# Kernel tuning notes

Measured on AMD Instinct MI355X. Metric: run time of the kernel, lower is better.

Reference implementation:

```python
import jax, jax.numpy as jnp
import numpy as np

N = 50000   # nodes per modality sub-graph
M = 20000   # hyperedges per modality
E = 200000  # incidences per modality
D = 128     # kg_emb_dim
H = 8       # mha_n_heads
C = 64      # context entities
NE = 200000 # n_entity


def hyper_conv(x, theta, bias, node_idx, edge_idx, num_edges):
    """PyG HypergraphConv (no attention): out = D^-1 H B^-1 H^T (X Theta) + b."""
    xt = x @ theta                                   # [N, D]
    n = x.shape[0]
    ones = jnp.ones(node_idx.shape, dtype=xt.dtype)
    B = jax.ops.segment_sum(ones, edge_idx, num_segments=num_edges)   # edge degree [M]
    Dn = jax.ops.segment_sum(ones, node_idx, num_segments=n)          # node degree [N]
    Binv = jnp.where(B > 0, 1.0 / B, 0.0)
    Dinv = jnp.where(Dn > 0, 1.0 / Dn, 0.0)
    e = jax.ops.segment_sum(xt[node_idx], edge_idx, num_segments=num_edges) * Binv[:, None]
    out = jax.ops.segment_sum(e[edge_idx], node_idx, num_segments=n) * Dinv[:, None]
    return out + bias


def mha(q_in, kv, wq, bq, wk, bk, wv, bv, wo, bo, n_heads):
    """torch.nn.MultiheadAttention(batch_first) with batch=1: query=[C,D], kv=[R,D]."""
    c, d = q_in.shape
    r = kv.shape[0]
    hd = d // n_heads
    q = (q_in @ wq + bq).reshape(c, n_heads, hd).transpose(1, 0, 2)   # [H,C,hd]
    k = (kv @ wk + bk).reshape(r, n_heads, hd).transpose(1, 0, 2)     # [H,R,hd]
    v = (kv @ wv + bv).reshape(r, n_heads, hd).transpose(1, 0, 2)     # [H,R,hd]
    scores = jnp.einsum('hcd,hrd->hcr', q, k) / jnp.sqrt(jnp.asarray(hd, q.dtype))
    attn = jax.nn.softmax(scores, axis=-1)
    o = jnp.einsum('hcr,hrd->hcd', attn, v)                           # [H,C,hd]
    o = o.transpose(1, 0, 2).reshape(c, d)
    return o @ wo + bo


def setup_inputs() -> dict:
    key = jax.random.key(0)
    ks = jax.random.split(key, 24)
    s = D ** -0.5
    inp = {
        'x_item': jax.random.normal(ks[0], (N, D), jnp.float32) * s,
        'theta_item': jax.random.normal(ks[1], (D, D), jnp.float32) * s,
        'bias_item': jnp.zeros((D,), jnp.float32),
        'x_ent': jax.random.normal(ks[2], (N, D), jnp.float32) * s,
        'theta_ent': jax.random.normal(ks[3], (D, D), jnp.float32) * s,
        'bias_ent': jnp.zeros((D,), jnp.float32),
        'x_word': jax.random.normal(ks[4], (N, D), jnp.float32) * s,
        'theta_word': jax.random.normal(ks[5], (D, D), jnp.float32) * s,
        'bias_word': jnp.zeros((D,), jnp.float32),
        'context': jax.random.normal(ks[6], (C, D), jnp.float32),
        'wq': jax.random.normal(ks[7], (D, D), jnp.float32) * s,
        'bq': jnp.zeros((D,), jnp.float32),
        'wk': jax.random.normal(ks[8], (D, D), jnp.float32) * s,
        'bk': jnp.zeros((D,), jnp.float32),
        'wv': jax.random.normal(ks[9], (D, D), jnp.float32) * s,
        'bv': jnp.zeros((D,), jnp.float32),
        'wo': jax.random.normal(ks[10], (D, D), jnp.float32) * s,
        'bo': jnp.zeros((D,), jnp.float32),
        'w_rec': jax.random.normal(ks[11], (D, NE), jnp.float32) * s,
        'b_rec': jnp.zeros((NE,), jnp.float32),
        'node_item': jax.random.randint(ks[12], (E,), 0, N, jnp.int32),
        'edge_item': jax.random.randint(ks[13], (E,), 0, M, jnp.int32),
        'node_ent': jax.random.randint(ks[14], (E,), 0, N, jnp.int32),
        'edge_ent': jax.random.randint(ks[15], (E,), 0, M, jnp.int32),
        'node_word': jax.random.randint(ks[16], (E,), 0, N, jnp.int32),
        'edge_word': jax.random.randint(ks[17], (E,), 0, M, jnp.int32),
        'num_edges': M,
    }
    return inp


def reference(x_item, theta_item, bias_item, x_ent, theta_ent, bias_ent,
              x_word, theta_word, bias_word, context,
              wq, bq, wk, bk, wv, bv, wo, bo, w_rec, b_rec,
              node_item, edge_item, node_ent, edge_ent, node_word, edge_word,
              num_edges):
    # Hypergraph conv per modality (item / entity / word sub-graphs)
    item_emb = hyper_conv(x_item, theta_item, bias_item, node_item, edge_item, num_edges)
    ent_emb = hyper_conv(x_ent, theta_ent, bias_ent, node_ent, edge_ent, num_edges)
    word_emb = hyper_conv(x_word, theta_word, bias_word, node_word, edge_word, num_edges)
    # related = cat(session_embedding, knowledge_embedding) across modalities
    related = jnp.concatenate([item_emb, ent_emb, word_emb], axis=0)   # [3N, D]
    # MHItemAttention: MHA(context, related, related)
    attentive = mha(context, related, wq, bq, wk, bk, wv, bv, wo, bo, H)  # [C, D]
    # Mean pooling path of _attention_and_gating
    user_repr = jnp.mean(attentive, axis=0)                            # [D]
    user_repr = jnp.mean(jnp.concatenate([context, user_repr[None]], axis=0), axis=0)
    # rec_bias: Linear(kg_emb_dim, n_entity)
    scores = user_repr @ w_rec + b_rec                                 # [n_entity]
    return scores
```

## Files before the change

### kernel.cpp

```cpp
#include <hip/hip_runtime.h>
#include <hip/hip_bf16.h>

constexpr int N_NODES = 50000;
constexpr int M_EDGES = 20000;
constexpr int E_INC   = 200000;
constexpr int H_HEADS = 8;
constexpr int C_CTX   = 64;
constexpr int NE_OUT  = 200000;
constexpr int R_REL   = 3 * N_NODES;

constexpr int STRIPS  = 128;
constexpr int SROWS   = 1172;

constexpr int CAP_E = 40;
constexpr int CAP_N = 24;

typedef short bf8v __attribute__((ext_vector_type(8)));
typedef float f4v  __attribute__((ext_vector_type(4)));
#define MFMA16(a, b, c) __builtin_amdgcn_mfma_f32_16x16x32_bf16(a, b, c, 0, 0, 0)

__device__ __forceinline__ unsigned short bfs(float f) {
    union { __hip_bfloat16 b; unsigned short s; } u;
    u.b = __float2bfloat16(f);
    return u.s;
}
__device__ __forceinline__ unsigned bfp(float lo, float hi) {
    union { __hip_bfloat162 b; unsigned u; } v;
    v.b = __float22bfloat162_rn(make_float2(lo, hi));
    return v.u;
}

__device__ __forceinline__ void gload16(const void* g, const void* l) {
    __builtin_amdgcn_global_load_lds(
        (const __attribute__((address_space(1))) void*)(unsigned long long)(size_t)g,
        (__attribute__((address_space(3))) void*)(unsigned)(size_t)l,
        16, 0, 0);
}

__global__ __launch_bounds__(256) void zero_kernel(float4* p, int n4) {
    int i = blockIdx.x * 256 + threadIdx.x;
    if (i < n4) p[i] = make_float4(0.f, 0.f, 0.f, 0.f);
}

__global__ __launch_bounds__(256) void wconv_kernel(
    const float* __restrict__ t0, const float* __restrict__ t1,
    const float* __restrict__ t2, unsigned short* __restrict__ out)
{
    int idx = blockIdx.x * 256 + threadIdx.x;
    int m = idx >> 14, p = idx & 16383;
    int n = p >> 7, k = p & 127;
    const float* src = (m == 0) ? t0 : (m == 1) ? t1 : t2;
    out[idx] = bfs(src[k * 128 + n]);
}

__global__ __launch_bounds__(256) void qkf_kernel(
    const float* __restrict__ ctx, const float* __restrict__ wq,
    const float* __restrict__ bq, const float* __restrict__ wk,
    const float* __restrict__ bk, unsigned short* __restrict__ qkb,
    float* __restrict__ cb)
{
    __shared__ float qrow[128];
    const int c = blockIdx.x, t = threadIdx.x;
    if (t < 128) {
        float s = bq[t];
        for (int k = 0; k < 128; ++k) s += ctx[c * 128 + k] * wq[(size_t)k * 128 + t];
        qrow[t] = s;
    }
    __syncthreads();
#pragma unroll
    for (int i = 0; i < 4; ++i) {
        int idx = t + i * 256;
        int h = idx >> 7, j = idx & 127;
        const float* wr = wk + (size_t)j * 128 + h * 16;
        const float* qr = qrow + h * 16;
        float s = 0.f;
#pragma unroll
        for (int d = 0; d < 16; ++d) s += qr[d] * wr[d];
        qkb[(size_t)(h * 64 + c) * 128 + j] = bfs(0.25f * s);
    }
    if (t < 8) {
        float s = 0.f;
#pragma unroll
        for (int d = 0; d < 16; ++d) s += qrow[t * 16 + d] * bk[t * 16 + d];
        cb[t * 64 + c] = 0.25f * s;
    }
}

__global__ __launch_bounds__(256) void xg_kernel(
    const float* __restrict__ x0, const float* __restrict__ x1,
    const float* __restrict__ x2, const unsigned short* __restrict__ thT,
    unsigned short* __restrict__ y, int R)
{
    int m = blockIdx.y;
    const float* X = (m == 0) ? x0 : (m == 1) ? x1 : x2;
    const unsigned short* W = thT + m * 16384;
    unsigned short* Y = y + (size_t)m * R * 128;
    const int w = threadIdx.x >> 6, lane = threadIdx.x & 63;
    const int ln15 = lane & 15, l16 = lane >> 4;
    const int r0 = blockIdx.x * 128 + w * 32;

    f4v acc[2][8];
#pragma unroll
    for (int i = 0; i < 2; ++i)
#pragma unroll
        for (int j = 0; j < 8; ++j) acc[i][j] = (f4v)0.f;

    for (int ks = 0; ks < 4; ++ks) {
        bf8v a[2];
#pragma unroll
        for (int mt = 0; mt < 2; ++mt) {
            int row = r0 + mt * 16 + ln15;
            row = (row < R) ? row : (R - 1);
            const float* xp = X + (size_t)row * 128 + ks * 32 + l16 * 8;
            float4 f0 = *(const float4*)xp;
            float4 f1 = *(const float4*)(xp + 4);
            union { bf8v v; unsigned w[4]; } u;
            u.w[0] = bfp(f0.x, f0.y);
            u.w[1] = bfp(f0.z, f0.w);
            u.w[2] = bfp(f1.x, f1.y);
            u.w[3] = bfp(f1.z, f1.w);
            a[mt] = u.v;
        }
#pragma unroll
        for (int nt = 0; nt < 8; ++nt) {
            bf8v b = *(const bf8v*)(W + (nt * 16 + ln15) * 128 + ks * 32 + l16 * 8);
            acc[0][nt] = MFMA16(a[0], b, acc[0][nt]);
            acc[1][nt] = MFMA16(a[1], b, acc[1][nt]);
        }
    }
#pragma unroll
    for (int mt = 0; mt < 2; ++mt)
#pragma unroll
        for (int reg = 0; reg < 4; ++reg) {
            int row = r0 + mt * 16 + l16 * 4 + reg;
            if (row < R) {
#pragma unroll
                for (int nt = 0; nt < 8; ++nt)
                    Y[(size_t)row * 128 + nt * 16 + ln15] = bfs(acc[mt][nt][reg]);
            }
        }
}

__global__ __launch_bounds__(256) void fillx_kernel(
    const int* __restrict__ n0, const int* __restrict__ e0,
    const int* __restrict__ n1, const int* __restrict__ e1,
    const int* __restrict__ n2, const int* __restrict__ e2,
    unsigned short* __restrict__ listE, unsigned short* __restrict__ listN,
    int* __restrict__ cnt)
{
    const int m = blockIdx.y;
    const int* nodeA = (m == 0) ? n0 : (m == 1) ? n1 : n2;
    const int* edgeA = (m == 0) ? e0 : (m == 1) ? e1 : e2;
    unsigned short* LE = listE + (size_t)m * M_EDGES * CAP_E;
    unsigned short* LN = listN + (size_t)m * N_NODES * CAP_N;
    int* cntE = cnt + m * M_EDGES;
    int* cntN = cnt + 3 * M_EDGES + m * N_NODES;

    int i0 = (blockIdx.x * 256 + threadIdx.x) * 4;
    if (i0 >= E_INC) return;
    int4 ev = *(const int4*)(edgeA + i0);
    int4 nv = *(const int4*)(nodeA + i0);
    int e[4] = {ev.x, ev.y, ev.z, ev.w};
    int n[4] = {nv.x, nv.y, nv.z, nv.w};
    int se[4], sn[4];
#pragma unroll
    for (int k = 0; k < 4; ++k) se[k] = atomicAdd(&cntE[e[k]], 1);
#pragma unroll
    for (int k = 0; k < 4; ++k) sn[k] = atomicAdd(&cntN[n[k]], 1);
#pragma unroll
    for (int k = 0; k < 4; ++k)
        if (se[k] < CAP_E) LE[(size_t)e[k] * CAP_E + se[k]] = (unsigned short)n[k];
#pragma unroll
    for (int k = 0; k < 4; ++k)
        if (sn[k] < CAP_N) LN[(size_t)n[k] * CAP_N + sn[k]] = (unsigned short)e[k];
}

#define ACC8(v) do { \
    a0 += __uint_as_float((v).x << 16); a1 += __uint_as_float((v).x & 0xFFFF0000u); \
    a2 += __uint_as_float((v).y << 16); a3 += __uint_as_float((v).y & 0xFFFF0000u); \
    a4 += __uint_as_float((v).z << 16); a5 += __uint_as_float((v).z & 0xFFFF0000u); \
    a6 += __uint_as_float((v).w << 16); a7 += __uint_as_float((v).w & 0xFFFF0000u); } while (0)

__global__ __launch_bounds__(256) void gedge_kernel(
    const unsigned short* __restrict__ xt,
    const unsigned short* __restrict__ listE, const int* __restrict__ cnt,
    unsigned short* __restrict__ eb)
{
    int mm = blockIdx.y;
    const unsigned short* X = xt + (size_t)mm * N_NODES * 128;
    unsigned short* Eo = eb + (size_t)mm * M_EDGES * 128;
    int t = blockIdx.x * 256 + threadIdx.x;
    int e = t >> 4, lane = t & 15;
    if (e >= M_EDGES) return;
    const unsigned short* seg = listE + ((size_t)mm * M_EDGES + e) * CAP_E;
    int deg = cnt[mm * M_EDGES + e];
    int en = (deg < CAP_E) ? deg : CAP_E;
    float a0 = 0, a1 = 0, a2 = 0, a3 = 0, a4 = 0, a5 = 0, a6 = 0, a7 = 0;
    int j = 0;
    for (; j + 8 <= en; j += 8) {
        int n0 = seg[j], n1 = seg[j + 1], n2 = seg[j + 2], n3 = seg[j + 3];
        int n4 = seg[j + 4], n5 = seg[j + 5], n6 = seg[j + 6], n7 = seg[j + 7];
        uint4 v0 = *(const uint4*)(X + (size_t)n0 * 128 + lane * 8);
        uint4 v1 = *(const uint4*)(X + (size_t)n1 * 128 + lane * 8);
        uint4 v2 = *(const uint4*)(X + (size_t)n2 * 128 + lane * 8);
        uint4 v3 = *(const uint4*)(X + (size_t)n3 * 128 + lane * 8);
        uint4 v4 = *(const uint4*)(X + (size_t)n4 * 128 + lane * 8);
        uint4 v5 = *(const uint4*)(X + (size_t)n5 * 128 + lane * 8);
        uint4 v6 = *(const uint4*)(X + (size_t)n6 * 128 + lane * 8);
        uint4 v7 = *(const uint4*)(X + (size_t)n7 * 128 + lane * 8);
        ACC8(v0); ACC8(v1); ACC8(v2); ACC8(v3);
        ACC8(v4); ACC8(v5); ACC8(v6); ACC8(v7);
    }
    for (; j + 4 <= en; j += 4) {
        int n0 = seg[j], n1 = seg[j + 1], n2 = seg[j + 2], n3 = seg[j + 3];
        uint4 v0 = *(const uint4*)(X + (size_t)n0 * 128 + lane * 8);
        uint4 v1 = *(const uint4*)(X + (size_t)n1 * 128 + lane * 8);
        uint4 v2 = *(const uint4*)(X + (size_t)n2 * 128 + lane * 8);
        uint4 v3 = *(const uint4*)(X + (size_t)n3 * 128 + lane * 8);
        ACC8(v0); ACC8(v1); ACC8(v2); ACC8(v3);
    }
    for (; j < en; ++j) {
        int n = seg[j];
        uint4 v = *(const uint4*)(X + (size_t)n * 128 + lane * 8);
        ACC8(v);
    }
    float bi = (deg > 0) ? 1.f / (float)deg : 0.f;
    uint4 o;
    o.x = bfp(a0 * bi, a1 * bi);
    o.y = bfp(a2 * bi, a3 * bi);
    o.z = bfp(a4 * bi, a5 * bi);
    o.w = bfp(a6 * bi, a7 * bi);
    *(uint4*)(Eo + (size_t)e * 128 + lane * 8) = o;
}

__global__ __launch_bounds__(256) void gnode_kernel(
    const unsigned short* __restrict__ eb,
    const unsigned short* __restrict__ listN, const int* __restrict__ cnt,
    const float* __restrict__ b0, const float* __restrict__ b1,
    const float* __restrict__ b2, unsigned short* __restrict__ rel)
{
    int mm = blockIdx.y;
    const unsigned short* E = eb + (size_t)mm * M_EDGES * 128;
    const float* bias = (mm == 0) ? b0 : (mm == 1) ? b1 : b2;
    unsigned short* R = rel + (size_t)mm * N_NODES * 128;
    int t = blockIdx.x * 256 + threadIdx.x;
    int n = t >> 4, lane = t & 15;
    if (n >= N_NODES) return;
    const unsigned short* seg = listN + ((size_t)mm * N_NODES + n) * CAP_N;
    int deg = cnt[3 * M_EDGES + mm * N_NODES + n];
    int en = (deg < CAP_N) ? deg : CAP_N;
    float a0 = 0, a1 = 0, a2 = 0, a3 = 0, a4 = 0, a5 = 0, a6 = 0, a7 = 0;
    int j = 0;
    for (; j + 4 <= en; j += 4) {
        int e0 = seg[j], e1 = seg[j + 1], e2 = seg[j + 2], e3 = seg[j + 3];
        uint4 v0 = *(const uint4*)(E + (size_t)e0 * 128 + lane * 8);
        uint4 v1 = *(const uint4*)(E + (size_t)e1 * 128 + lane * 8);
        uint4 v2 = *(const uint4*)(E + (size_t)e2 * 128 + lane * 8);
        uint4 v3 = *(const uint4*)(E + (size_t)e3 * 128 + lane * 8);
        ACC8(v0); ACC8(v1); ACC8(v2); ACC8(v3);
    }
    for (; j < en; ++j) {
        int e = seg[j];
        uint4 v = *(const uint4*)(E + (size_t)e * 128 + lane * 8);
        ACC8(v);
    }
    float di = (deg > 0) ? 1.f / (float)deg : 0.f;
    uint4 o;
    o.x = bfp(a0 * di + bias[lane * 8 + 0], a1 * di + bias[lane * 8 + 1]);
    o.y = bfp(a2 * di + bias[lane * 8 + 2], a3 * di + bias[lane * 8 + 3]);
    o.z = bfp(a4 * di + bias[lane * 8 + 4], a5 * di + bias[lane * 8 + 5]);
    o.w = bfp(a6 * di + bias[lane * 8 + 6], a7 * di + bias[lane * 8 + 7]);
    *(uint4*)(R + (size_t)n * 128 + lane * 8) = o;
}

__global__ __launch_bounds__(256) void attn_kernel(
    const unsigned short* __restrict__ rel, const unsigned short* __restrict__ qkb,
    const float* __restrict__ cb, float* __restrict__ PRpart, float* __restrict__ lpart)
{
    __shared__ __align__(16) unsigned char relN[2][16384];
    __shared__ __align__(16) unsigned char relTb[16384];
    __shared__ __align__(16) unsigned char Plb[16384];

    const int strip = blockIdx.x, pair = blockIdx.y;
    const int t = threadIdx.x, w = t >> 6, lane = t & 63;
    const int ln15 = lane & 15, l16 = lane >> 4;
    const int aswz = (ln15 & 7) << 4;

    bf8v bq[2][4];
#pragma unroll
    for (int nt = 0; nt < 2; ++nt)
#pragma unroll
        for (int ks = 0; ks < 4; ++ks)
            bq[nt][ks] = *(const bf8v*)(qkb +
                (size_t)(pair * 128 + w * 32 + nt * 16 + ln15) * 128 + ks * 32 + l16 * 8);
    float cbr[2];
#pragma unroll
    for (int nt = 0; nt < 2; ++nt)
        cbr[nt] = cb[pair * 128 + w * 32 + nt * 16 + ln15];

    f4v pr[2][8];
#pragma unroll
    for (int i = 0; i < 2; ++i)
#pragma unroll
        for (int j = 0; j < 8; ++j) pr[i][j] = (f4v)0.f;
    float lacc[2] = {0.f, 0.f};

    const int r0s = strip * SROWS;
    const int rend = (r0s + SROWS < R_REL) ? (r0s + SROWS) : R_REL;
    const int nchunk = (rend - r0s + 63) >> 6;

    auto stage = [&](int base, int b) {
#pragma unroll
        for (int k = 0; k < 4; ++k) {
            int o = k * 4096 + w * 1024 + lane * 16;
            int rr = o >> 8;
            int cbyte = (o & 255) ^ ((rr & 7) << 4);
            gload16(rel + (size_t)(base + rr) * 128 + (cbyte >> 1),
                    &relN[b][k * 4096 + w * 1024]);
        }
    };

    stage(r0s, 0);
    int cur = 0;
    for (int c = 0; c < nchunk; ++c) {
        const int base = r0s + c * 64;
        const int nvalid = rend - base;

        if (c + 1 < nchunk) {
            stage(base + 64, cur ^ 1);
            __builtin_amdgcn_sched_barrier(0);
            asm volatile("s_waitcnt vmcnt(4)" ::: "memory");
        } else {
            __builtin_amdgcn_sched_barrier(0);
            asm volatile("s_waitcnt vmcnt(0)" ::: "memory");
        }
        __builtin_amdgcn_sched_barrier(0);
        __builtin_amdgcn_s_barrier();
        __builtin_amdgcn_sched_barrier(0);

        const unsigned char* RN = relN[cur];

#pragma unroll
        for (int a2 = 0; a2 < 2; ++a2) {
            int idx = t + a2 * 256;
            int rp = idx & 31, jg = idx >> 5;
            int r2 = rp * 2;
            uint4 A = *(const uint4*)(RN + r2 * 256 + ((jg * 16) ^ ((r2 & 7) << 4)));
            uint4 B = *(const uint4*)(RN + (r2 + 1) * 256 + ((jg * 16) ^ (((r2 + 1) & 7) << 4)));
            unsigned aw[4] = {A.x, A.y, A.z, A.w};
            unsigned bw[4] = {B.x, B.y, B.z, B.w};
#pragma unroll
            for (int jj = 0; jj < 4; ++jj) {
                int j0 = jg * 8 + jj * 2;
                *(unsigned*)(relTb + j0 * 128 + ((rp * 4) ^ ((jj * 2) << 4))) =
                    (aw[jj] & 0xFFFFu) | (bw[jj] << 16);
                *(unsigned*)(relTb + (j0 + 1) * 128 + ((rp * 4) ^ ((jj * 2 + 1) << 4))) =
                    (aw[jj] >> 16) | (bw[jj] & 0xFFFF0000u);
            }
        }

        f4v sc[4][2];
#pragma unroll
        for (int i = 0; i < 4; ++i) { sc[i][0] = (f4v)0.f; sc[i][1] = (f4v)0.f; }
        __builtin_amdgcn_s_setprio(1);
#pragma unroll
        for (int ks = 0; ks < 4; ++ks) {
            bf8v a[4];
#pragma unroll
            for (int mt = 0; mt < 4; ++mt)
                a[mt] = *(const bf8v*)(RN + (mt * 16 + ln15) * 256 +
                                       ((ks * 64 + l16 * 16) ^ aswz));
#pragma unroll
            for (int mt = 0; mt < 4; ++mt) {
                sc[mt][0] = MFMA16(a[mt], bq[0][ks], sc[mt][0]);
                sc[mt][1] = MFMA16(a[mt], bq[1][ks], sc[mt][1]);
            }
        }
        __builtin_amdgcn_s_setprio(0);

        bool full = (nvalid >= 64);
#pragma unroll
        for (int nt = 0; nt < 2; ++nt) {
            float ls = 0.f;
#pragma unroll
            for (int mt = 0; mt < 4; ++mt) {
                float pv[4];
#pragma unroll
                for (int reg = 0; reg < 4; ++reg) {
                    int rl = mt * 16 + l16 * 4 + reg;
                    float p = __expf(sc[mt][nt][reg] + cbr[nt]);
                    if (!full && rl >= nvalid) p = 0.f;
                    ls += p;
                    pv[reg] = p;
                }
                int hc = w * 32 + nt * 16 + ln15;
                int pb = hc * 128 + ((mt * 32 + l16 * 8) ^ aswz);
                *(uint2*)(Plb + pb) = make_uint2(bfp(pv[0], pv[1]), bfp(pv[2], pv[3]));
            }
            ls += __shfl_xor(ls, 16, 64);
            ls += __shfl_xor(ls, 32, 64);
            lacc[nt] += ls;
        }

        asm volatile("s_waitcnt lgkmcnt(0)" ::: "memory");
        __builtin_amdgcn_sched_barrier(0);
        __builtin_amdgcn_s_barrier();
        __builtin_amdgcn_sched_barrier(0);

        __builtin_amdgcn_s_setprio(1);
#pragma unroll
        for (int ks = 0; ks < 2; ++ks) {
            bf8v ap[2];
#pragma unroll
            for (int mt = 0; mt < 2; ++mt) {
                int hc = w * 32 + mt * 16 + ln15;
                ap[mt] = *(const bf8v*)(Plb + hc * 128 + ((ks * 64 + l16 * 16) ^ aswz));
            }
#pragma unroll
            for (int nt = 0; nt < 8; ++nt) {
                int j = nt * 16 + ln15;
                bf8v b = *(const bf8v*)(relTb + j * 128 + ((ks * 64 + l16 * 16) ^ aswz));
                pr[0][nt] = MFMA16(ap[0], b, pr[0][nt]);
                pr[1][nt] = MFMA16(ap[1], b, pr[1][nt]);
            }
        }
        __builtin_amdgcn_s_setprio(0);
        cur ^= 1;
    }

    float* PB = PRpart + (size_t)(pair * STRIPS + strip) * 128 * 128;
#pragma unroll
    for (int mt = 0; mt < 2; ++mt)
#pragma unroll
        for (int reg = 0; reg < 4; ++reg) {
            int hcl = w * 32 + mt * 16 + l16 * 4 + reg;
#pragma unroll
            for (int nt = 0; nt < 8; ++nt)
                PB[hcl * 128 + nt * 16 + ln15] = pr[mt][nt][reg];
        }
    if (lane < 16) {
        float* LB = lpart + (size_t)(pair * STRIPS + strip) * 128;
        LB[w * 32 + ln15] = lacc[0];
        LB[w * 32 + 16 + ln15] = lacc[1];
    }
}

__global__ __launch_bounds__(256) void reduce_kernel(
    const float* __restrict__ PRpart, const float* __restrict__ lpart,
    const float* __restrict__ wv, const float* __restrict__ bv,
    float* __restrict__ osum)
{
    int hc = blockIdx.x;
    int pair = hc >> 7, hcl = hc & 127, h = hc >> 6;
    __shared__ float PS[128];
    __shared__ float LL[129];
    int t = threadIdx.x;
    if (t < 128) {
        float s = 0.f;
        const float* p = PRpart + ((size_t)(pair * STRIPS) * 128 + hcl) * 128 + t;
        for (int st = 0; st < STRIPS; ++st) s += p[(size_t)st * 128 * 128];
        PS[t] = s;
    } else {
        int idx = t - 128;
        LL[idx] = lpart[(size_t)(pair * STRIPS + idx) * 128 + hcl];
    }
    __syncthreads();
    if (t == 0) {
        float l = 0.f;
        for (int st = 0; st < 128; ++st) l += LL[st];
        LL[128] = l;
    }
    __syncthreads();
    if (t < 16) {
        float o = 0.f;
        for (int j = 0; j < 128; ++j) o += PS[j] * wv[(size_t)j * 128 + h * 16 + t];
        float on = o / LL[128] + bv[h * 16 + t];
        atomicAdd(&osum[h * 16 + t], on);
    }
}

__global__ __launch_bounds__(128) void user_kernel(
    const float* __restrict__ ctx, const float* __restrict__ osum,
    const float* __restrict__ wo, const float* __restrict__ bo,
    float* __restrict__ u)
{
    __shared__ float os[128];
    int d = threadIdx.x;
    os[d] = osum[d];
    __syncthreads();
    float cs = 0.f;
    for (int cc = 0; cc < 64; ++cc) cs += ctx[cc * 128 + d];
    float ow = 0.f;
    for (int j = 0; j < 128; ++j) ow += os[j] * wo[j * 128 + d];
    u[d] = (cs + ow * (1.f / 64.f) + bo[d]) * (1.f / 65.f);
}

__global__ __launch_bounds__(256) void rec_kernel(
    const float* __restrict__ u, const float* __restrict__ wrec,
    const float* __restrict__ brec, float* __restrict__ out)
{
    __shared__ float ul[128];
    if (threadIdx.x < 128) ul[threadIdx.x] = u[threadIdx.x];
    __syncthreads();
    int j = blockIdx.x * 256 + threadIdx.x;
    if (j >= NE_OUT) return;
    float a0 = brec[j], a1 = 0.f, a2 = 0.f, a3 = 0.f;
#pragma unroll 4
    for (int d = 0; d < 128; d += 4) {
        a0 += ul[d + 0] * wrec[(size_t)(d + 0) * NE_OUT + j];
        a1 += ul[d + 1] * wrec[(size_t)(d + 1) * NE_OUT + j];
        a2 += ul[d + 2] * wrec[(size_t)(d + 2) * NE_OUT + j];
        a3 += ul[d + 3] * wrec[(size_t)(d + 3) * NE_OUT + j];
    }
    out[j] = (a0 + a1) + (a2 + a3);
}

extern "C" void kernel_launch(void* const* d_in, const int* in_sizes, int n_in,
                              void* d_out, int out_size, void* d_ws, size_t ws_size,
                              hipStream_t stream)
{
    const float* ctx  = (const float*)d_in[9];
    const float* wq = (const float*)d_in[10];
    const float* bq = (const float*)d_in[11];
    const float* wk = (const float*)d_in[12];
    const float* bk = (const float*)d_in[13];
    const float* wv = (const float*)d_in[14];
    const float* bv = (const float*)d_in[15];
    const float* wo = (const float*)d_in[16];
    const float* bo = (const float*)d_in[17];
    const float* wrec = (const float*)d_in[18];
    const float* brec = (const float*)d_in[19];
    const int* node0 = (const int*)d_in[20];
    const int* edge0 = (const int*)d_in[21];
    const int* node1 = (const int*)d_in[22];
    const int* edge1 = (const int*)d_in[23];
    const int* node2 = (const int*)d_in[24];
    const int* edge2 = (const int*)d_in[25];
    float* out = (float*)d_out;

    char* ws = (char*)d_ws;
    size_t off = 0;
    auto alloc = [&](size_t nbytes) {
        void* p = ws + off;
        off += (nbytes + 255) & ~(size_t)255;
        return p;
    };
    unsigned short* rel  = (unsigned short*)alloc((size_t)R_REL * 128 * 2);
    unsigned short* xt   = (unsigned short*)alloc((size_t)3 * N_NODES * 128 * 2);
    unsigned short* eb   = (unsigned short*)alloc((size_t)3 * M_EDGES * 128 * 2);
    float* PRpart = (float*)alloc((size_t)4 * STRIPS * 128 * 128 * 4);
    float* lpart  = (float*)alloc((size_t)4 * STRIPS * 128 * 4);
    unsigned short* qkb = (unsigned short*)alloc(512 * 128 * 2);
    float* cbv    = (float*)alloc(512 * 4);
    unsigned short* thT = (unsigned short*)alloc(3 * 16384 * 2);
    int* cnt      = (int*)alloc((size_t)(3 * M_EDGES + 3 * N_NODES + 128) * 4);
    float* osum   = (float*)(cnt + 3 * M_EDGES + 3 * N_NODES);
    unsigned short* listE = (unsigned short*)alloc((size_t)3 * M_EDGES * CAP_E * 2);
    unsigned short* listN = (unsigned short*)alloc((size_t)3 * N_NODES * CAP_N * 2);
    float* u      = (float*)alloc(128 * 4);
    (void)ws_size; (void)in_sizes; (void)n_in; (void)out_size;

    {
        int nwords = 3 * M_EDGES + 3 * N_NODES + 128;
        zero_kernel<<<(nwords / 4 + 255) / 256, 256, 0, stream>>>((float4*)cnt, nwords / 4);
    }
    fillx_kernel<<<dim3((E_INC / 4 + 255) / 256, 3), 256, 0, stream>>>(
        node0, edge0, node1, edge1, node2, edge2, listE, listN, cnt);
    wconv_kernel<<<192, 256, 0, stream>>>((const float*)d_in[1], (const float*)d_in[4],
                                          (const float*)d_in[7], thT);
    qkf_kernel<<<64, 256, 0, stream>>>(ctx, wq, bq, wk, bk, qkb, cbv);
    xg_kernel<<<dim3((N_NODES + 127) / 128, 3), 256, 0, stream>>>(
        (const float*)d_in[0], (const float*)d_in[3], (const float*)d_in[6], thT, xt, N_NODES);
    gedge_kernel<<<dim3(M_EDGES * 16 / 256, 3), 256, 0, stream>>>(xt, listE, cnt, eb);
    gnode_kernel<<<dim3(N_NODES * 16 / 256, 3), 256, 0, stream>>>(
        eb, listN, cnt, (const float*)d_in[2], (const float*)d_in[5],
        (const float*)d_in[8], rel);
    attn_kernel<<<dim3(STRIPS, 4), 256, 0, stream>>>(rel, qkb, cbv, PRpart, lpart);
    reduce_kernel<<<512, 256, 0, stream>>>(PRpart, lpart, wv, bv, osum);
    user_kernel<<<1, 128, 0, stream>>>(ctx, osum, wo, bo, u);
    rec_kernel<<<(NE_OUT + 255) / 256, 256, 0, stream>>>(u, wrec, brec, out);
}
```

Baseline: 490.0 us.

## Partition incidence-list build by XCD slice to localize atomics in L2

The incidence-list fill kernel now assigns each block to one of eight edge/node index slices, chosen by blockIdx modulo 8 to match round-robin XCD dispatch. Each block scans a chunk of incidences and only does atomics and list writes for indices in its slice, so the counters for a given slice stay in one XCD's L2. This trades eight-fold redundant reads of the index arrays, plus branch divergence, for less cross-die coherence traffic on the atomics.

```diff
diff --git a/kernel.cpp b/kernel.cpp
--- a/kernel.cpp
+++ b/kernel.cpp
@@ -14,6 +14,12 @@
 
 constexpr int CAP_E = 40;
 constexpr int CAP_N = 24;
+
+constexpr int NXCD   = 8;
+constexpr int SL_E   = M_EDGES / NXCD;
+constexpr int SL_N   = N_NODES / NXCD;
+constexpr int FCH    = 85;
+constexpr int FCHUNK = (E_INC + FCH - 1) / FCH;
 
 typedef short bf8v __attribute__((ext_vector_type(8)));
 typedef float f4v  __attribute__((ext_vector_type(4)));
@@ -148,7 +154,12 @@
     unsigned short* __restrict__ listE, unsigned short* __restrict__ listN,
     int* __restrict__ cnt)
 {
-    const int m = blockIdx.y;
+    const int gid = blockIdx.x;
+    const int slice = gid & 7;
+    const int rest = gid >> 3;
+    const int m = rest % 3;
+    const int c = rest / 3;
+
     const int* nodeA = (m == 0) ? n0 : (m == 1) ? n1 : n2;
     const int* edgeA = (m == 0) ? e0 : (m == 1) ? e1 : e2;
     unsigned short* LE = listE + (size_t)m * M_EDGES * CAP_E;
@@ -156,23 +167,22 @@
     int* cntE = cnt + m * M_EDGES;
     int* cntN = cnt + 3 * M_EDGES + m * N_NODES;
 
-    int i0 = (blockIdx.x * 256 + threadIdx.x) * 4;
-    if (i0 >= E_INC) return;
-    int4 ev = *(const int4*)(edgeA + i0);
-    int4 nv = *(const int4*)(nodeA + i0);
-    int e[4] = {ev.x, ev.y, ev.z, ev.w};
-    int n[4] = {nv.x, nv.y, nv.z, nv.w};
-    int se[4], sn[4];
-#pragma unroll
-    for (int k = 0; k < 4; ++k) se[k] = atomicAdd(&cntE[e[k]], 1);
-#pragma unroll
-    for (int k = 0; k < 4; ++k) sn[k] = atomicAdd(&cntN[n[k]], 1);
-#pragma unroll
-    for (int k = 0; k < 4; ++k)
-        if (se[k] < CAP_E) LE[(size_t)e[k] * CAP_E + se[k]] = (unsigned short)n[k];
-#pragma unroll
-    for (int k = 0; k < 4; ++k)
-        if (sn[k] < CAP_N) LN[(size_t)n[k] * CAP_N + sn[k]] = (unsigned short)e[k];
+    const int eLo = slice * SL_E, nLo = slice * SL_N;
+    const int start = c * FCHUNK;
+    const int end = (start + FCHUNK < E_INC) ? (start + FCHUNK) : E_INC;
+
+    for (int i = start + threadIdx.x; i < end; i += 256) {
+        int e = edgeA[i];
+        int n = nodeA[i];
+        if ((unsigned)(e - eLo) < (unsigned)SL_E) {
+            int s = atomicAdd(&cntE[e], 1);
+            if (s < CAP_E) LE[(size_t)e * CAP_E + s] = (unsigned short)n;
+        }
+        if ((unsigned)(n - nLo) < (unsigned)SL_N) {
+            int s = atomicAdd(&cntN[n], 1);
+            if (s < CAP_N) LN[(size_t)n * CAP_N + s] = (unsigned short)e;
+        }
+    }
 }
 
 #define ACC8(v) do { \
@@ -564,7 +574,7 @@
         int nwords = 3 * M_EDGES + 3 * N_NODES + 128;
         zero_kernel<<<(nwords / 4 + 255) / 256, 256, 0, stream>>>((float4*)cnt, nwords / 4);
     }
-    fillx_kernel<<<dim3((E_INC / 4 + 255) / 256, 3), 256, 0, stream>>>(
+    fillx_kernel<<<NXCD * 3 * FCH, 256, 0, stream>>>(
         node0, edge0, node1, edge1, node2, edge2, listE, listN, cnt);
     wconv_kernel<<<192, 256, 0, stream>>>((const float*)d_in[1], (const float*)d_in[4],
                                           (const float*)d_in[7], thT);
```

New measurement: 468.4 us. 1.05x faster.
